# Kernel optimization log

Hardware: AMD Instinct MI355X
Metric: run time of the kernel (lower is better)

## Reference

```python
import jax, jax.numpy as jnp
import numpy as np

B, S, D_MODEL, HEADS = 2, 2048, 1024, 16
K_D = D_MODEL // HEADS


def setup_inputs() -> dict:
    key = jax.random.key(0)
    ks = jax.random.split(key, 5)
    x = jax.random.normal(ks[0], (B, S, D_MODEL), dtype=jnp.float32)
    # causal mask, 1 = keep, 0 = masked (GPT-2 style)
    mask = jnp.tril(jnp.ones((S, S), dtype=jnp.int32))[None, None, :, :]
    sc = 0.02
    w_attn = jax.random.normal(ks[1], (D_MODEL, 3 * D_MODEL), dtype=jnp.float32) * sc
    b_attn = jax.random.normal(ks[2], (3 * D_MODEL,), dtype=jnp.float32) * sc
    w_proj = jax.random.normal(ks[3], (D_MODEL, D_MODEL), dtype=jnp.float32) * sc
    b_proj = jax.random.normal(ks[4], (D_MODEL,), dtype=jnp.float32) * sc
    return {"x": x, "mask": mask, "w_attn": w_attn, "b_attn": b_attn,
            "w_proj": w_proj, "b_proj": b_proj}


def reference(x, mask, w_attn, b_attn, w_proj, b_proj):
    b, s, _ = x.shape
    qkv = x @ w_attn + b_attn                      # [B,S,3*d_model]
    # NOTE: source assigns value, query, key = split(...) in that order
    v, q, k = jnp.split(qkv, 3, axis=-1)
    def heads(t):  # [B,S,d_model] -> [B,H,S,k_d]
        return t.reshape(b, s, HEADS, K_D).transpose(0, 2, 1, 3)
    v, q, k = heads(v), heads(q), heads(k)
    present = jnp.stack((k, v))                    # [2,B,H,S,k_d]
    scores = jnp.einsum('bhqd,bhkd->bhqk', q, k) / jnp.sqrt(jnp.float32(K_D))
    scores = jnp.where(mask == 0, -jnp.inf, scores)
    attn = jax.nn.softmax(scores, axis=-1)         # [B,H,S,S]
    out = jnp.einsum('bhqk,bhkd->bhqd', attn, v)   # [B,H,S,k_d]
    out = out.transpose(0, 2, 1, 3).reshape(b, s, D_MODEL)
    out = out @ w_proj + b_proj
    return out, present
```

## Files before the change

kernel.cpp:

```cpp
#include <hip/hip_runtime.h>
#include <math.h>

constexpr int BB = 2;
constexpr int SS = 2048;
constexpr int DM = 1024;
constexpr int NH = 16;
constexpr int KD = 64;
constexpr int OUT_ELEMS  = BB*SS*DM;
constexpr int PRES_HALF  = BB*NH*SS*KD;
#define NEGSENT (-1e30f)

typedef __attribute__((ext_vector_type(8))) short short8;
typedef __attribute__((ext_vector_type(4))) short short4v;
typedef __attribute__((ext_vector_type(4))) float f32x4;

__device__ __forceinline__ float us2f(unsigned short u) {
  union { unsigned int ui; float f; } c; c.ui = ((unsigned int)u) << 16; return c.f;
}
__device__ __forceinline__ short f2s(float f) {
  union { float f; unsigned int u; } c; c.f = f;
  return (short)((c.u + 0x7FFFu + ((c.u >> 16) & 1u)) >> 16);
}
__device__ __forceinline__ short f2s_hw(float f) {
  unsigned int r;
  asm("v_cvt_pk_bf16_f32 %0, %1, %1" : "=v"(r) : "v"(f));
  return (short)r;
}

#define GLOAD_LDS16(g, l) \
  __builtin_amdgcn_global_load_lds((const __attribute__((address_space(1))) void*)(g), \
                                   (__attribute__((address_space(3))) void*)(l), 16, 0, 0)

__global__ __launch_bounds__(256)
void cast_x_k(const float* __restrict__ x, short* __restrict__ xb) {
  const size_t i = ((size_t)blockIdx.x * 256 + threadIdx.x) * 4;
  const float4 v = *(const float4*)(x + i);
  short4v s; s.x = f2s(v.x); s.y = f2s(v.y); s.z = f2s(v.z); s.w = f2s(v.w);
  *(short4v*)(xb + i) = s;
}

__global__ __launch_bounds__(256)
void transpose_k(const float* __restrict__ w, int N, short* __restrict__ wt) {
  __shared__ float tl[32][33];
  const int tx = threadIdx.x & 31, ty = threadIdx.x >> 5;
  const int n0 = blockIdx.x * 32, k0 = blockIdx.y * 32;
  #pragma unroll
  for (int i = 0; i < 4; ++i) {
    const int kk = ty + i * 8;
    tl[kk][tx] = w[(size_t)(k0 + kk) * N + n0 + tx];
  }
  __syncthreads();
  #pragma unroll
  for (int i = 0; i < 4; ++i) {
    const int nn = ty + i * 8;
    wt[(size_t)(n0 + nn) * 1024 + k0 + tx] = f2s(tl[tx][nn]);
  }
}

__global__ __launch_bounds__(256)
void v_tr_k(const float* __restrict__ vf, short* __restrict__ vt) {
  __shared__ float tl[64][65];
  const int bh = blockIdx.x;
  const int s0 = blockIdx.y * 64;
  const int tr = threadIdx.x >> 2;
  const int tc = (threadIdx.x & 3) * 16;
  const float* src = vf + ((size_t)bh * SS + s0) * KD;
  #pragma unroll
  for (int i = 0; i < 4; ++i) {
    const float4 v = *(const float4*)(src + (size_t)tr * KD + tc + i * 4);
    tl[tr][tc + i * 4 + 0] = v.x; tl[tr][tc + i * 4 + 1] = v.y;
    tl[tr][tc + i * 4 + 2] = v.z; tl[tr][tc + i * 4 + 3] = v.w;
  }
  __syncthreads();
  short8 o0, o1;
  #pragma unroll
  for (int i = 0; i < 8; ++i) o0[i] = f2s(tl[tc + i][tr]);
  #pragma unroll
  for (int i = 0; i < 8; ++i) o1[i] = f2s(tl[tc + 8 + i][tr]);
  short* dst = vt + ((size_t)bh * KD + tr) * SS + s0 + tc;
  *(short8*)(dst) = o0;
  *(short8*)(dst + 8) = o1;
}

__device__ __forceinline__ void mfma_tile_loop(
    const short* __restrict__ A, const short* __restrict__ Bt,
    int m0, int n0, short* Asm, short* Bsm, f32x4 (*acc)[4]) {
  const int tid = threadIdx.x;
  const int lane = tid & 63;
  const int w = tid >> 6;
  const int wm = (w >> 1) * 64, wn = (w & 1) * 64;
  const int ln15 = lane & 15, quad = lane >> 4;
  for (int k0 = 0; k0 < 1024; k0 += 32) {
    #pragma unroll
    for (int j = 0; j < 2; ++j) {
      const int e = j * 256 + tid;
      const int r = e >> 2, cq = e & 3;
      GLOAD_LDS16(A  + (size_t)(m0 + r) * 1024 + k0 + cq * 8, Asm + e * 8);
      GLOAD_LDS16(Bt + (size_t)(n0 + r) * 1024 + k0 + cq * 8, Bsm + e * 8);
    }
    __syncthreads();
    short8 af[4], bf[4];
    #pragma unroll
    for (int t = 0; t < 4; ++t)
      af[t] = *(const short8*)(Asm + (wm + t * 16 + ln15) * 32 + quad * 8);
    #pragma unroll
    for (int t = 0; t < 4; ++t)
      bf[t] = *(const short8*)(Bsm + (wn + t * 16 + ln15) * 32 + quad * 8);
    #pragma unroll
    for (int tm = 0; tm < 4; ++tm)
      #pragma unroll
      for (int tn = 0; tn < 4; ++tn)
        acc[tm][tn] = __builtin_amdgcn_mfma_f32_16x16x32_bf16(
            af[tm], bf[tn], acc[tm][tn], 0, 0, 0);
    __syncthreads();
  }
}

__global__ __launch_bounds__(256)
void qkv_mfma_k(const short* __restrict__ A, const short* __restrict__ Bt,
                const float* __restrict__ bias, short* __restrict__ qbf,
                float* __restrict__ outf, short* __restrict__ kbf) {
  __shared__ short Asm[128 * 32];
  __shared__ short Bsm[128 * 32];
  const int n0 = blockIdx.x * 128, m0 = blockIdx.y * 128;
  f32x4 acc[4][4] = {};
  mfma_tile_loop(A, Bt, m0, n0, Asm, Bsm, acc);
  const int lane = threadIdx.x & 63;
  const int w = threadIdx.x >> 6;
  const int wm = (w >> 1) * 64, wn = (w & 1) * 64;
  const int col = lane & 15, row4 = (lane >> 4) * 4;
  #pragma unroll
  for (int tm = 0; tm < 4; ++tm) {
    #pragma unroll
    for (int tn = 0; tn < 4; ++tn) {
      const int n = n0 + wn + tn * 16 + col;
      #pragma unroll
      for (int r = 0; r < 4; ++r) {
        const int m = m0 + wm + tm * 16 + row4 + r;
        const float val = acc[tm][tn][r] + bias[n];
        const int bb = m >> 11, s = m & 2047;
        const int c = n & 1023, h = c >> 6, d = c & 63;
        const size_t idx = ((size_t)(bb * NH + h) * SS + s) * KD + d;
        if (n < DM) {
          outf[(size_t)OUT_ELEMS + (size_t)PRES_HALF + idx] = val;
        } else if (n < 2 * DM) {
          qbf[idx] = f2s(val);
        } else {
          outf[(size_t)OUT_ELEMS + idx] = val;
          if (kbf) kbf[idx] = f2s(val);
        }
      }
    }
  }
}

__global__ __launch_bounds__(256)
void proj_mfma_k(const short* __restrict__ A, const short* __restrict__ Bt,
                 const float* __restrict__ bias, float* __restrict__ outf) {
  __shared__ short Asm[128 * 32];
  __shared__ short Bsm[128 * 32];
  const int n0 = blockIdx.x * 128, m0 = blockIdx.y * 128;
  f32x4 acc[4][4] = {};
  mfma_tile_loop(A, Bt, m0, n0, Asm, Bsm, acc);
  const int lane = threadIdx.x & 63;
  const int w = threadIdx.x >> 6;
  const int wm = (w >> 1) * 64, wn = (w & 1) * 64;
  const int col = lane & 15, row4 = (lane >> 4) * 4;
  #pragma unroll
  for (int tm = 0; tm < 4; ++tm) {
    #pragma unroll
    for (int tn = 0; tn < 4; ++tn) {
      const int n = n0 + wn + tn * 16 + col;
      const float b = bias[n];
      #pragma unroll
      for (int r = 0; r < 4; ++r) {
        const int m = m0 + wm + tm * 16 + row4 + r;
        outf[(size_t)m * DM + n] = acc[tm][tn][r] + b;
      }
    }
  }
}

__device__ __forceinline__ void stage_kv4(const short* __restrict__ Kg,
                                          const short* __restrict__ Vg,
                                          int kb, short* Ksb, short* Vtb,
                                          int tid) {
  #pragma unroll
  for (int rd = 0; rd < 2; ++rd) {
    const int i = rd * 256 + tid;
    const int row = i >> 3, grp = i & 7;
    const int sw = (grp ^ (row & 7)) << 3;
    GLOAD_LDS16(Kg + (size_t)(kb + row) * KD + sw, Ksb + i * 8);
    GLOAD_LDS16(Vg + (size_t)row * SS + kb + sw, Vtb + i * 8);
  }
}

__global__ __launch_bounds__(256)
void attn_mfma8_k(const short* __restrict__ qbf, const short* __restrict__ kbf,
                  const short* __restrict__ vbft, short* __restrict__ obf) {
  __shared__ short Ks[2][64 * 64];
  __shared__ short Vt[2][64 * 64];
  __shared__ short Ps[4][16 * 64];
  const int bid = blockIdx.x;
  const int xcd = bid & 7, g = bid >> 3;
  const int rnd = g >> 4;
  const int p   = g & 15;
  const int bh  = (xcd << 2) | rnd;
  const int tid = threadIdx.x;
  const int w   = tid >> 6;
  const int lane = tid & 63;
  const int ln15 = lane & 15, quad = lane >> 4;
  const int rswz = (ln15 & 7) << 3;
  const float SC2 = 0.125f * 1.44269504f;
  const float THR = 8.0f;

  const short* Kg = kbf  + (size_t)bh * SS * KD;
  const short* Vg = vbft + (size_t)bh * KD * SS;
  short* Pw = Ps[w];
  const int bb = bh >> 4, h = bh & 15;

  #pragma unroll 1
  for (int pass = 0; pass < 2; ++pass) {
    const int qb = pass ? (31 - p) : p;
    const int q0 = qb * 64;
    const int nch = qb + 1;

    short8 aq[2];
    {
      const short* qp = qbf + ((size_t)bh * SS + q0 + w * 16) * KD;
      aq[0] = *(const short8*)(qp + (size_t)ln15 * KD + quad * 8);
      aq[1] = *(const short8*)(qp + (size_t)ln15 * KD + 32 + quad * 8);
    }
    f32x4 O[4] = {};
    float mreg[4], lreg[4];
    #pragma unroll
    for (int r = 0; r < 4; ++r) { mreg[r] = NEGSENT; lreg[r] = 0.f; }

    stage_kv4(Kg, Vg, 0, Ks[0], Vt[0], tid);
    __syncthreads();

    for (int ch = 0; ch < nch; ++ch) {
      const int cur = ch & 1;
      if (ch + 1 < nch)
        stage_kv4(Kg, Vg, (ch + 1) * 64, Ks[cur ^ 1], Vt[cur ^ 1], tid);
      const short* Kc = Ks[cur];
      const short* Vc = Vt[cur];

      f32x4 S[4] = {};
      #pragma unroll
      for (int kt = 0; kt < 2; ++kt) {
        short8 bk[4];
        #pragma unroll
        for (int tn = 0; tn < 4; ++tn)
          bk[tn] = *(const short8*)(Kc + (tn * 16 + ln15) * 64 + ((kt * 32 + quad * 8) ^ rswz));
        #pragma unroll
        for (int tn = 0; tn < 4; ++tn)
          S[tn] = __builtin_amdgcn_mfma_f32_16x16x32_bf16(aq[kt], bk[tn], S[tn], 0, 0, 0);
      }

      if (ch == qb) {
        const int rowl = w * 16 + quad * 4;
        #pragma unroll
        for (int tn = 0; tn < 4; ++tn) {
          const int colk = tn * 16 + ln15;
          #pragma unroll
          for (int r = 0; r < 4; ++r)
            if (colk > rowl + r) S[tn][r] = NEGSENT;
        }
      }

      {
        float lmax = S[0][0];
        #pragma unroll
        for (int tn = 0; tn < 4; ++tn)
          #pragma unroll
          for (int r = 0; r < 4; ++r) lmax = fmaxf(lmax, S[tn][r]);
        const float mmin = fminf(fminf(mreg[0], mreg[1]), fminf(mreg[2], mreg[3]));
        const bool ok = (lmax - mmin) <= THR;
        if (!__all((int)ok)) {
          #pragma unroll
          for (int r = 0; r < 4; ++r) {
            float mx = fmaxf(fmaxf(fmaxf(S[0][r], S[1][r]), S[2][r]), S[3][r]);
            mx = fmaxf(mx, __shfl_xor(mx, 1, 64));
            mx = fmaxf(mx, __shfl_xor(mx, 2, 64));
            mx = fmaxf(mx, __shfl_xor(mx, 4, 64));
            mx = fmaxf(mx, __shfl_xor(mx, 8, 64));
            const float mn = fmaxf(mreg[r], mx);
            const float al = exp2f((mreg[r] - mn) * SC2);
            mreg[r] = mn;
            lreg[r] *= al;
            O[0][r] *= al; O[1][r] *= al; O[2][r] *= al; O[3][r] *= al;
          }
        }
      }

      #pragma unroll
      for (int r = 0; r < 4; ++r) {
        const float mnsc = mreg[r] * SC2;
        const int prow = quad * 4 + r;
        const int rs = (prow & 7) << 3;
        float p0 = exp2f(fmaf(S[0][r], SC2, -mnsc));
        float p1 = exp2f(fmaf(S[1][r], SC2, -mnsc));
        float p2 = exp2f(fmaf(S[2][r], SC2, -mnsc));
        float p3 = exp2f(fmaf(S[3][r], SC2, -mnsc));
        lreg[r] += (p0 + p1) + (p2 + p3);
        Pw[prow * 64 + ((0 * 16 + ln15) ^ rs)] = f2s_hw(p0);
        Pw[prow * 64 + ((1 * 16 + ln15) ^ rs)] = f2s_hw(p1);
        Pw[prow * 64 + ((2 * 16 + ln15) ^ rs)] = f2s_hw(p2);
        Pw[prow * 64 + ((3 * 16 + ln15) ^ rs)] = f2s_hw(p3);
      }
      asm volatile("s_waitcnt lgkmcnt(0)" ::: "memory");
      __builtin_amdgcn_sched_barrier(0);

      #pragma unroll
      for (int kt = 0; kt < 2; ++kt) {
        short8 ap = *(const short8*)(Pw + ln15 * 64 + ((kt * 32 + quad * 8) ^ rswz));
        short8 bv[4];
        #pragma unroll
        for (int tn = 0; tn < 4; ++tn)
          bv[tn] = *(const short8*)(Vc + (tn * 16 + ln15) * 64 + ((kt * 32 + quad * 8) ^ rswz));
        #pragma unroll
        for (int tn = 0; tn < 4; ++tn)
          O[tn] = __builtin_amdgcn_mfma_f32_16x16x32_bf16(ap, bv[tn], O[tn], 0, 0, 0);
      }
      __syncthreads();
    }

    #pragma unroll
    for (int r = 0; r < 4; ++r) {
      float l = lreg[r];
      l += __shfl_xor(l, 1, 64);
      l += __shfl_xor(l, 2, 64);
      l += __shfl_xor(l, 4, 64);
      l += __shfl_xor(l, 8, 64);
      lreg[r] = 1.f / fmaxf(l, 1e-30f);
    }
    short* ob = obf + ((size_t)bb * SS + q0 + w * 16) * DM + h * KD;
    #pragma unroll
    for (int tn = 0; tn < 4; ++tn)
      #pragma unroll
      for (int r = 0; r < 4; ++r)
        ob[(size_t)(quad * 4 + r) * DM + tn * 16 + ln15] = f2s_hw(O[tn][r] * lreg[r]);
  }
}

__global__ __launch_bounds__(256)
void attn_k(const short* __restrict__ qbf, const float* __restrict__ pres,
            short* __restrict__ obf) {
  __shared__ float Ksf[32][64];
  __shared__ float Vsf[32][64];
  const int bh = blockIdx.x;
  const int q0 = ((int)gridDim.y - 1 - (int)blockIdx.y) * 64;
  const int t  = threadIdx.x;
  const int part = t & 3;
  const int row  = t >> 2;
  const int qr   = q0 + row;
  const int dbase = part * 16;
  const size_t qoff = ((size_t)bh * SS + qr) * KD + dbase;
  float q[16], o[16];
  #pragma unroll
  for (int i = 0; i < 16; ++i) q[i] = us2f((unsigned short)qbf[qoff + i]);
  #pragma unroll
  for (int i = 0; i < 16; ++i) o[i] = 0.f;
  float m = NEGSENT, l = 0.f;
  const float* Kb = pres + (size_t)bh * SS * KD;
  const float* Vb = pres + (size_t)PRES_HALF + (size_t)bh * SS * KD;
  const int nch = (q0 + 64) / 32;
  for (int ch = 0; ch < nch; ++ch) {
    const int kbase = ch * 32;
    __syncthreads();
    {
      const float4* ksrc = (const float4*)(Kb + (size_t)kbase * KD);
      const float4* vsrc = (const float4*)(Vb + (size_t)kbase * KD);
      float4* kdst = (float4*)&Ksf[0][0];
      float4* vdst = (float4*)&Vsf[0][0];
      #pragma unroll
      for (int i = 0; i < 2; ++i) {
        kdst[t + i * 256] = ksrc[t + i * 256];
        vdst[t + i * 256] = vsrc[t + i * 256];
      }
    }
    __syncthreads();
    float sc[32];
    #pragma unroll
    for (int kk = 0; kk < 32; ++kk) {
      float s = 0.f;
      #pragma unroll
      for (int i = 0; i < 16; ++i) s = fmaf(q[i], Ksf[kk][dbase + i], s);
      s += __shfl_xor(s, 1, 64);
      s += __shfl_xor(s, 2, 64);
      sc[kk] = (kbase + kk <= qr) ? s * 0.125f : NEGSENT;
    }
    float mc = sc[0];
    #pragma unroll
    for (int kk = 1; kk < 32; ++kk) mc = fmaxf(mc, sc[kk]);
    const float mn = fmaxf(m, mc);
    const float alpha = __expf(m - mn);
    l *= alpha;
    #pragma unroll
    for (int i = 0; i < 16; ++i) o[i] *= alpha;
    #pragma unroll
    for (int kk = 0; kk < 32; ++kk) {
      const float p = __expf(sc[kk] - mn);
      l += p;
      #pragma unroll
      for (int i = 0; i < 16; ++i) o[i] = fmaf(p, Vsf[kk][dbase + i], o[i]);
    }
    m = mn;
  }
  const float inv = 1.f / fmaxf(l, 1e-30f);
  const int bb = bh >> 4, h = bh & 15;
  const size_t ooff = ((size_t)(bb * SS + qr)) * DM + h * KD + dbase;
  #pragma unroll
  for (int i = 0; i < 16; ++i) obf[ooff + i] = f2s(o[i] * inv);
}

extern "C" void kernel_launch(void* const* d_in, const int* in_sizes, int n_in,
                              void* d_out, int out_size, void* d_ws, size_t ws_size,
                              hipStream_t stream) {
  const float* x      = (const float*)d_in[0];
  const float* w_attn = (const float*)d_in[2];
  const float* b_attn = (const float*)d_in[3];
  const float* w_proj = (const float*)d_in[4];
  const float* b_proj = (const float*)d_in[5];
  float* outf = (float*)d_out;

  constexpr size_t MB = 1024 * 1024;
  if (ws_size >= 24 * MB) {
    short* ws0   = (short*)d_ws;
    short* x_bf  = ws0;
    short* o_bf  = ws0;
    short* wat_t = ws0 + (size_t)4 * 1024 * 1024;
    short* wpt_t = ws0 + (size_t)7 * 1024 * 1024;
    short* q_bf  = ws0 + (size_t)8 * 1024 * 1024;
    short* k_bf  = (short*)d_out;
    short* v_bft = k_bf + (size_t)PRES_HALF;

    cast_x_k<<<4096, 256, 0, stream>>>(x, x_bf);
    transpose_k<<<dim3(96, 32), 256, 0, stream>>>(w_attn, 3 * DM, wat_t);
    transpose_k<<<dim3(32, 32), 256, 0, stream>>>(w_proj, DM, wpt_t);

    qkv_mfma_k<<<dim3(24, 32), 256, 0, stream>>>(x_bf, wat_t, b_attn, q_bf, outf,
                                                 k_bf);

    v_tr_k<<<dim3(BB * NH, SS / 64), 256, 0, stream>>>(
        outf + OUT_ELEMS + PRES_HALF, v_bft);

    attn_mfma8_k<<<dim3(512), 256, 0, stream>>>(q_bf, k_bf, v_bft, o_bf);

    proj_mfma_k<<<dim3(8, 32), 256, 0, stream>>>(o_bf, wpt_t, b_proj, outf);
  } else {
    short* x_bf;
    short* q_bf;
    short* wat_t;
    short* wpt_t;
    short* o_bf;
    if (ws_size >= 16 * MB) {
      short* ws = (short*)d_ws;
      x_bf  = (short*)d_out;
      q_bf  = x_bf + OUT_ELEMS;
      wat_t = ws;
      wpt_t = wat_t + 3 * DM * DM;
      o_bf  = wat_t + 4 * DM * DM;
    } else {
      x_bf  = (short*)d_out;
      q_bf  = x_bf + OUT_ELEMS;
      wat_t = (short*)d_in[1];
      wpt_t = wat_t + 3 * DM * DM;
      o_bf  = wat_t + 4 * DM * DM;
    }
    cast_x_k<<<4096, 256, 0, stream>>>(x, x_bf);
    transpose_k<<<dim3(96, 32), 256, 0, stream>>>(w_attn, 3 * DM, wat_t);
    transpose_k<<<dim3(32, 32), 256, 0, stream>>>(w_proj, DM, wpt_t);
    qkv_mfma_k<<<dim3(24, 32), 256, 0, stream>>>(x_bf, wat_t, b_attn, q_bf, outf,
                                                 nullptr);
    attn_k<<<dim3(BB * NH, SS / 64), 256, 0, stream>>>(q_bf, outf + OUT_ELEMS, o_bf);
    proj_mfma_k<<<dim3(8, 32), 256, 0, stream>>>(o_bf, wpt_t, b_proj, outf);
  }
}
```

Baseline: 226.7 us.

## Merge prep kernels into one launch and pack P stores with permuted V keys

Fuses the x cast and the two weight transposes into a single prep kernel dispatched by block index, removing two launches. In attention, P values are now converted two at a time with v_cvt_pk_bf16_f32 and written as 32-bit LDS stores. This changes the column order of P, so the V transpose kernel permutes key positions to match. The permutation has to line up exactly with the MFMA operand layout, or the attention output will be wrong.

```diff
diff --git a/kernel.cpp b/kernel.cpp
--- a/kernel.cpp
+++ b/kernel.cpp
@@ -26,24 +26,35 @@
   asm("v_cvt_pk_bf16_f32 %0, %1, %1" : "=v"(r) : "v"(f));
   return (short)r;
 }
+__device__ __forceinline__ unsigned int pk2(float lo, float hi) {
+  unsigned int r;
+  asm("v_cvt_pk_bf16_f32 %0, %1, %2" : "=v"(r) : "v"(lo), "v"(hi));
+  return r;
+}
 
 #define GLOAD_LDS16(g, l) \
   __builtin_amdgcn_global_load_lds((const __attribute__((address_space(1))) void*)(g), \
                                    (__attribute__((address_space(3))) void*)(l), 16, 0, 0)
 
 __global__ __launch_bounds__(256)
-void cast_x_k(const float* __restrict__ x, short* __restrict__ xb) {
-  const size_t i = ((size_t)blockIdx.x * 256 + threadIdx.x) * 4;
-  const float4 v = *(const float4*)(x + i);
-  short4v s; s.x = f2s(v.x); s.y = f2s(v.y); s.z = f2s(v.z); s.w = f2s(v.w);
-  *(short4v*)(xb + i) = s;
-}
-
-__global__ __launch_bounds__(256)
-void transpose_k(const float* __restrict__ w, int N, short* __restrict__ wt) {
+void prep_k(const float* __restrict__ x, short* __restrict__ xb,
+            const float* __restrict__ wa, short* __restrict__ wat,
+            const float* __restrict__ wp, short* __restrict__ wpt) {
   __shared__ float tl[32][33];
+  const int bid = blockIdx.x;
+  if (bid < 4096) {
+    const size_t i = ((size_t)bid * 256 + threadIdx.x) * 4;
+    const float4 v = *(const float4*)(x + i);
+    short4v s; s.x = f2s(v.x); s.y = f2s(v.y); s.z = f2s(v.z); s.w = f2s(v.w);
+    *(short4v*)(xb + i) = s;
+    return;
+  }
+  const float* w; short* wt; int N, t;
+  if (bid < 4096 + 3072) { w = wa; wt = wat; N = 3 * DM; t = bid - 4096;
+  } else { w = wp; wt = wpt; N = DM; t = bid - 7168; }
+  const int nb = (N == DM) ? 32 : 96;
+  const int n0 = (t % nb) * 32, k0 = (t / nb) * 32;
   const int tx = threadIdx.x & 31, ty = threadIdx.x >> 5;
-  const int n0 = blockIdx.x * 32, k0 = blockIdx.y * 32;
   #pragma unroll
   for (int i = 0; i < 4; ++i) {
     const int kk = ty + i * 8;
@@ -74,9 +85,17 @@
   __syncthreads();
   short8 o0, o1;
   #pragma unroll
-  for (int i = 0; i < 8; ++i) o0[i] = f2s(tl[tc + i][tr]);
-  #pragma unroll
-  for (int i = 0; i < 8; ++i) o1[i] = f2s(tl[tc + 8 + i][tr]);
+  for (int i = 0; i < 8; ++i) {
+    const int pos = tc + i;
+    const int key = (pos & 32) | ((pos & 31) >> 1) | ((pos & 1) << 4);
+    o0[i] = f2s(tl[key][tr]);
+  }
+  #pragma unroll
+  for (int i = 0; i < 8; ++i) {
+    const int pos = tc + 8 + i;
+    const int key = (pos & 32) | ((pos & 31) >> 1) | ((pos & 1) << 4);
+    o1[i] = f2s(tl[key][tr]);
+  }
   short* dst = vt + ((size_t)bh * KD + tr) * SS + s0 + tc;
   *(short8*)(dst) = o0;
   *(short8*)(dst + 8) = o1;
@@ -196,7 +215,7 @@
 }
 
 __global__ __launch_bounds__(256)
-void attn_mfma8_k(const short* __restrict__ qbf, const short* __restrict__ kbf,
+void attn_mfma9_k(const short* __restrict__ qbf, const short* __restrict__ kbf,
                   const short* __restrict__ vbft, short* __restrict__ obf) {
   __shared__ short Ks[2][64 * 64];
   __shared__ short Vt[2][64 * 64];
@@ -304,10 +323,8 @@
         float p2 = exp2f(fmaf(S[2][r], SC2, -mnsc));
         float p3 = exp2f(fmaf(S[3][r], SC2, -mnsc));
         lreg[r] += (p0 + p1) + (p2 + p3);
-        Pw[prow * 64 + ((0 * 16 + ln15) ^ rs)] = f2s_hw(p0);
-        Pw[prow * 64 + ((1 * 16 + ln15) ^ rs)] = f2s_hw(p1);
-        Pw[prow * 64 + ((2 * 16 + ln15) ^ rs)] = f2s_hw(p2);
-        Pw[prow * 64 + ((3 * 16 + ln15) ^ rs)] = f2s_hw(p3);
+        *(unsigned int*)(Pw + prow * 64 + ((2 * ln15) ^ rs))      = pk2(p0, p1);
+        *(unsigned int*)(Pw + prow * 64 + ((32 + 2 * ln15) ^ rs)) = pk2(p2, p3);
       }
       asm volatile("s_waitcnt lgkmcnt(0)" ::: "memory");
       __builtin_amdgcn_sched_barrier(0);
@@ -436,9 +453,7 @@
     short* k_bf  = (short*)d_out;
     short* v_bft = k_bf + (size_t)PRES_HALF;
 
-    cast_x_k<<<4096, 256, 0, stream>>>(x, x_bf);
-    transpose_k<<<dim3(96, 32), 256, 0, stream>>>(w_attn, 3 * DM, wat_t);
-    transpose_k<<<dim3(32, 32), 256, 0, stream>>>(w_proj, DM, wpt_t);
+    prep_k<<<8192, 256, 0, stream>>>(x, x_bf, w_attn, wat_t, w_proj, wpt_t);
 
     qkv_mfma_k<<<dim3(24, 32), 256, 0, stream>>>(x_bf, wat_t, b_attn, q_bf, outf,
                                                  k_bf);
@@ -446,7 +461,7 @@
     v_tr_k<<<dim3(BB * NH, SS / 64), 256, 0, stream>>>(
         outf + OUT_ELEMS + PRES_HALF, v_bft);
 
-    attn_mfma8_k<<<dim3(512), 256, 0, stream>>>(q_bf, k_bf, v_bft, o_bf);
+    attn_mfma9_k<<<dim3(512), 256, 0, stream>>>(q_bf, k_bf, v_bft, o_bf);
 
     proj_mfma_k<<<dim3(8, 32), 256, 0, stream>>>(o_bf, wpt_t, b_proj, outf);
   } else {
@@ -469,9 +484,7 @@
       wpt_t = wat_t + 3 * DM * DM;
       o_bf  = wat_t + 4 * DM * DM;
     }
-    cast_x_k<<<4096, 256, 0, stream>>>(x, x_bf);
-    transpose_k<<<dim3(96, 32), 256, 0, stream>>>(w_attn, 3 * DM, wat_t);
-    transpose_k<<<dim3(32, 32), 256, 0, stream>>>(w_proj, DM, wpt_t);
+    prep_k<<<8192, 256, 0, stream>>>(x, x_bf, w_attn, wat_t, w_proj, wpt_t);
     qkv_mfma_k<<<dim3(24, 32), 256, 0, stream>>>(x_bf, wat_t, b_attn, q_bf, outf,
                                                  nullptr);
     attn_k<<<dim3(BB * NH, SS / 64), 256, 0, stream>>>(q_bf, outf + OUT_ELEMS, o_bf);
```

Result: faster. 219.3 us (-3.3%).
